# Optimization experiments

Measured on AMD Instinct MI355X. Metric: run time of the kernel, lower is better.

## Reference

```python
import jax, jax.numpy as jnp
import numpy as np

# LIF hyperparameters (match init_kwargs)
DT = 1.0
TAU = 20.0
THRESHOLD = 1.0
RESET = 0.0
REST = 0.0
REFR_PERIOD = 2.0
LOW_BOUND = -1.0
KOEFF = float(np.exp(-DT / TAU))  # membrane decay per step
N = 2048
N_IN = 512
N_OUT = 256
B = 64
T = 512


def setup_inputs() -> dict:
    key = jax.random.key(0)
    k1, k2 = jax.random.split(key)
    # Binary input spike trains [B, n_in, T] (uint8 semantics, stored as float32)
    inp = (jax.random.uniform(k1, (B, N_IN, T)) < 0.2).astype(jnp.float32)
    # Dense synaptic weight matrix W [N, N]; row i = incoming weights of neuron i
    W = jax.random.normal(k2, (N, N), dtype=jnp.float32) * (0.1 / np.sqrt(N))
    return {"inp": inp, "W": W}


def reference(inp, W):
    batch, n_in, time = inp.shape
    n = W.shape[0]
    xs = jnp.moveaxis(inp, 2, 0)  # [T, B, n_in]

    def step(carry, x_t):
        state, refr, out_t = carry  # state/refr/out_t: [B, N]
        # Inject input spikes into the first n_in output slots
        out_t = out_t.at[:, :n_in].set(x_t)
        # LIF update: decay toward rest + synaptic input W @ out_t
        state = (state - REST) * KOEFF + REST + jnp.einsum('ij,bj->bi', W, out_t)
        # Refractory neurons clamped to reset potential
        state = jnp.where(refr > 0, RESET, state)
        spike = state >= THRESHOLD
        refr = refr - DT
        refr = jnp.where(spike, REFR_PERIOD, refr)
        # Lower-bound clamp on membrane potential
        state = jnp.where(state < LOW_BOUND, LOW_BOUND, state)
        out_t = spike.astype(jnp.float32)
        return (state, refr, out_t), out_t[:, -N_OUT:]

    init = (jnp.zeros((batch, n), jnp.float32),
            jnp.zeros((batch, n), jnp.float32),
            jnp.zeros((batch, n), jnp.float32))
    _, outs = jax.lax.scan(step, init, xs)  # outs: [T, B, n_out]
    return jnp.transpose(outs, (1, 2, 0))  # [B, n_out, T]
```

## Files before the change

### kernel.cpp

```cpp
#include <hip/hip_runtime.h>

#define KOEFF 0.951229424500714f
#define K64   0.040762204f
#define LOG2K (-0.07213475204444817f)

typedef unsigned short u16;
typedef __attribute__((ext_vector_type(8))) short short8;
typedef __attribute__((ext_vector_type(4))) float f32x4;

__device__ __forceinline__ u16 f2bf(float f) {
  unsigned int v = __float_as_uint(f);
  unsigned int r = (v + 0x7FFFu + ((v >> 16) & 1u)) >> 16;
  return (u16)r;
}
__device__ __forceinline__ float bf2f(u16 u) {
  return __uint_as_float(((unsigned int)u) << 16);
}

__global__ __launch_bounds__(256) void k_prep(const float* __restrict__ X, const float* __restrict__ W,
                                              u16* __restrict__ XT, u16* __restrict__ Whi,
                                              float* __restrict__ WT2, int* __restrict__ flags) {
  __shared__ float tile[64][65];
  const int blk = blockIdx.x;
  if (blk < 4096) {
    const int b  = blk >> 6;
    const int r2 = blk & 63;
    const int j0 = (r2 & 7) * 64;
    const int t0 = (r2 >> 3) * 64;
    const float* src = X + ((size_t)b * 512 + j0) * 512 + t0;
    for (int e = threadIdx.x; e < 64 * 16; e += 256) {
      int r = e >> 4, c = e & 15;
      float4 v = *(const float4*)(src + (size_t)r * 512 + c * 4);
      tile[r][c * 4 + 0] = v.x; tile[r][c * 4 + 1] = v.y;
      tile[r][c * 4 + 2] = v.z; tile[r][c * 4 + 3] = v.w;
    }
    __syncthreads();
    u16* dst = XT + ((size_t)b * 512 + t0) * 512 + j0;
    for (int e = threadIdx.x; e < 64 * 16; e += 256) {
      int tr = e >> 4, c = e & 15;
      ushort4 o;
      o.x = f2bf(tile[c * 4 + 0][tr]); o.y = f2bf(tile[c * 4 + 1][tr]);
      o.z = f2bf(tile[c * 4 + 2][tr]); o.w = f2bf(tile[c * 4 + 3][tr]);
      *(ushort4*)(dst + (size_t)tr * 512 + c * 4) = o;
    }
  } else if (blk < 7168) {
    if (blk == 4096 && threadIdx.x < 64) flags[threadIdx.x] = 0;
    int p = (blk - 4096) * 256 + threadIdx.x;
    int i = p >> 9, j = p & 511;
    Whi[p] = f2bf(W[(size_t)(512 + i) * 2048 + j]);
  } else {
    const int bx = blk - 7168;
    const int i0 = (bx / 24) * 64;
    const int j0 = (bx % 24) * 64;
    const float* src = W + (size_t)(512 + i0) * 2048 + 512 + j0;
    for (int e = threadIdx.x; e < 64 * 16; e += 256) {
      int r = e >> 4, c = e & 15;
      float4 v = *(const float4*)(src + (size_t)r * 2048 + c * 4);
      tile[r][c * 4 + 0] = v.x; tile[r][c * 4 + 1] = v.y;
      tile[r][c * 4 + 2] = v.z; tile[r][c * 4 + 3] = v.w;
    }
    __syncthreads();
    float* dst = WT2 + (size_t)j0 * 1536 + i0;
    for (int e = threadIdx.x; e < 64 * 16; e += 256) {
      int jr = e >> 4, c = e & 15;
      float4 o;
      o.x = tile[c * 4 + 0][jr]; o.y = tile[c * 4 + 1][jr];
      o.z = tile[c * 4 + 2][jr]; o.w = tile[c * 4 + 3][jr];
      *(float4*)(dst + (size_t)jr * 1536 + c * 4) = o;
    }
  }
}

__global__ __launch_bounds__(256) void k_gemm(const u16* __restrict__ A,
                                              const u16* __restrict__ Bx, u16* __restrict__ U,
                                              float* __restrict__ P) {
  __shared__ u16 lA[128 * 64];
  __shared__ u16 lB[128 * 64];
  const int b    = blockIdx.y;
  const int mt   = blockIdx.x >> 2;
  const int nt   = blockIdx.x & 3;
  const int tid  = threadIdx.x;
  const int wv   = tid >> 6;
  const int lane = tid & 63;
  const int wr   = wv >> 1, wc = wv & 1;

  f32x4 acc[4][4];
#pragma unroll
  for (int mi = 0; mi < 4; ++mi)
#pragma unroll
    for (int ni = 0; ni < 4; ++ni) acc[mi][ni] = (f32x4)0.0f;

  const u16* gA = A + (size_t)mt * 128 * 512;
  const u16* gB = Bx + ((size_t)b * 512 + nt * 128) * 512;

  for (int k0 = 0; k0 < 512; k0 += 64) {
#pragma unroll
    for (int it = 0; it < 4; ++it) {
      int byteoff = wv * 4096 + it * 1024 + lane * 16;
      int row   = byteoff >> 7;
      int chunk = (byteoff >> 4) & 7;
      int ksub  = (chunk ^ (row & 7)) * 8;
      int ldsoff = wv * 2048 + it * 512;
      __builtin_amdgcn_global_load_lds(
          (const __attribute__((address_space(1))) void*)(gA + (size_t)row * 512 + k0 + ksub),
          (__attribute__((address_space(3))) void*)(lA + ldsoff), 16, 0, 0);
      __builtin_amdgcn_global_load_lds(
          (const __attribute__((address_space(1))) void*)(gB + (size_t)row * 512 + k0 + ksub),
          (__attribute__((address_space(3))) void*)(lB + ldsoff), 16, 0, 0);
    }
    __syncthreads();
#pragma unroll
    for (int kk = 0; kk < 2; ++kk) {
      short8 ah[4], bb[4];
      const int kc = kk * 4 + (lane >> 4);
      const int sw = lane & 7;
#pragma unroll
      for (int mi = 0; mi < 4; ++mi) {
        int m = wr * 64 + mi * 16 + (lane & 15);
        ah[mi] = *(const short8*)&lA[m * 64 + ((kc ^ sw) << 3)];
      }
#pragma unroll
      for (int ni = 0; ni < 4; ++ni) {
        int n = wc * 64 + ni * 16 + (lane & 15);
        bb[ni] = *(const short8*)&lB[n * 64 + ((kc ^ sw) << 3)];
      }
#pragma unroll
      for (int mi = 0; mi < 4; ++mi)
#pragma unroll
        for (int ni = 0; ni < 4; ++ni)
          acc[mi][ni] = __builtin_amdgcn_mfma_f32_16x16x32_bf16(ah[mi], bb[ni], acc[mi][ni], 0, 0, 0);
    }
    __syncthreads();
  }
#pragma unroll
  for (int mi = 0; mi < 4; ++mi) {
    int ib = mt * 128 + wr * 64 + mi * 16 + ((lane >> 4) << 2);
#pragma unroll
    for (int ni = 0; ni < 4; ++ni) {
      int t = nt * 128 + wc * 64 + ni * 16 + (lane & 15);
      f32x4 v = acc[mi][ni];
      ushort4 o;
      o.x = f2bf(v.x); o.y = f2bf(v.y); o.z = f2bf(v.z); o.w = f2bf(v.w);
      *(ushort4*)(U + ((size_t)b * 512 + t) * 1536 + ib) = o;
    }
  }
  {
    const int tl = lane & 15;
    const int c  = nt * 2 + wc;
    float pv[4][4];
#pragma unroll
    for (int mi = 0; mi < 4; ++mi)
#pragma unroll
      for (int q = 0; q < 4; ++q) pv[mi][q] = 0.f;
#pragma unroll
    for (int ni = 0; ni < 4; ++ni) {
      float w = exp2f(LOG2K * (float)(63 - ni * 16 - tl));
#pragma unroll
      for (int mi = 0; mi < 4; ++mi) {
        f32x4 a = acc[mi][ni];
        pv[mi][0] = fmaf(w, a.x, pv[mi][0]);
        pv[mi][1] = fmaf(w, a.y, pv[mi][1]);
        pv[mi][2] = fmaf(w, a.z, pv[mi][2]);
        pv[mi][3] = fmaf(w, a.w, pv[mi][3]);
      }
    }
#pragma unroll
    for (int off = 1; off < 16; off <<= 1)
#pragma unroll
      for (int mi = 0; mi < 4; ++mi)
#pragma unroll
        for (int q = 0; q < 4; ++q)
          pv[mi][q] += __shfl_xor(pv[mi][q], off, 16);
    if (tl == 0) {
      int ib = mt * 128 + wr * 64 + ((lane >> 4) << 2);
      float* pb = P + ((size_t)b * 8 + c) * 1536 + ib;
#pragma unroll
      for (int mi = 0; mi < 4; ++mi)
#pragma unroll
        for (int q = 0; q < 4; ++q) pb[mi * 16 + q] = pv[mi][q];
    }
  }
}

__global__ __launch_bounds__(256) void k_chunk(const u16* __restrict__ U, const float* __restrict__ P,
                                               float* __restrict__ out, int* __restrict__ flags) {
  const int g = blockIdx.x * 256 + threadIdx.x;
  const int i = g * 2;
  const int c = blockIdx.y, b = blockIdx.z;
  float s0 = 0.f, s1 = 0.f;
  const float* pp = P + (size_t)b * 8 * 1536 + i;
  for (int d = 0; d < c; ++d) {
    float2 pv = *(const float2*)(pp + (size_t)d * 1536);
    s0 = fmaf(s0, K64, pv.x);
    s1 = fmaf(s1, K64, pv.y);
  }
  const u16* up = U + ((size_t)b * 512 + c * 64) * 1536 + i;
  const bool wr = (i >= 1280);
  float* op = out + ((size_t)b * 256 + (i - 1280)) * 512 + c * 64;
  bool viol = false;
  unsigned int buf[8];
#pragma unroll
  for (int j = 0; j < 8; ++j) buf[j] = *(const unsigned int*)(up + (size_t)j * 1536);
  for (int t0 = 0; t0 < 64; t0 += 8) {
    float sp0[8], sp1[8];
#pragma unroll
    for (int j = 0; j < 8; ++j) {
      unsigned int u = buf[j];
      if (t0 + 8 < 64) buf[j] = *(const unsigned int*)(up + (size_t)(t0 + 8 + j) * 1536);
      s0 = fmaf(s0, KOEFF, bf2f((u16)(u & 0xffffu)));
      s1 = fmaf(s1, KOEFF, bf2f((u16)(u >> 16)));
      bool a = (s0 >= 1.0f), bsp = (s1 >= 1.0f);
      viol = viol || a || bsp || (s0 < -1.0f) || (s1 < -1.0f);
      sp0[j] = a ? 1.f : 0.f;
      sp1[j] = bsp ? 1.f : 0.f;
    }
    if (wr) {
      *(float4*)(op + t0)           = make_float4(sp0[0], sp0[1], sp0[2], sp0[3]);
      *(float4*)(op + t0 + 4)       = make_float4(sp0[4], sp0[5], sp0[6], sp0[7]);
      *(float4*)(op + 512 + t0)     = make_float4(sp1[0], sp1[1], sp1[2], sp1[3]);
      *(float4*)(op + 512 + t0 + 4) = make_float4(sp1[4], sp1[5], sp1[6], sp1[7]);
    }
  }
  if (viol) atomicOr(&flags[b], 1);
}

__global__ __launch_bounds__(768) void k_fix(const u16* __restrict__ U, const float* __restrict__ WT2,
                                             const int* __restrict__ flags, float* __restrict__ out) {
  const int b = blockIdx.x;
  if (flags[b] == 0) return;
  const int tid = threadIdx.x;
  const int wv = tid >> 6, lane = tid & 63;
  __shared__ unsigned long long spk[24];
  for (int w = tid; w < 24; w += 768) spk[w] = 0ULL;
  __syncthreads();
  float s0 = 0.f, s1 = 0.f, r0 = 0.f, r1 = 0.f;
  const int i0 = 2 * tid;
  const u16* ub = U + (size_t)b * 512 * 1536 + i0;
  unsigned int u = *(const unsigned int*)ub;
  for (int t = 0; t < 512; ++t) {
    unsigned int unext = u;
    if (t < 511) unext = *(const unsigned int*)(ub + (size_t)(t + 1) * 1536);
    float a0 = fmaf(s0, KOEFF, bf2f((u16)(u & 0xffffu)));
    float a1 = fmaf(s1, KOEFF, bf2f((u16)(u >> 16)));
    for (int wd = 0; wd < 24; ++wd) {
      unsigned long long m = spk[wd];
      while (m) {
        int bit = __ffsll(m) - 1;
        m &= m - 1;
        int jp = ((wd >> 1) << 7) + (bit << 1) + (wd & 1);
        float2 rv = *(const float2*)(WT2 + (size_t)jp * 1536 + i0);
        a0 += rv.x; a1 += rv.y;
      }
    }
    if (r0 > 0.f) a0 = 0.f;
    if (r1 > 0.f) a1 = 0.f;
    bool sp0 = a0 >= 1.0f, sp1 = a1 >= 1.0f;
    r0 -= 1.f; r1 -= 1.f;
    if (sp0) r0 = 2.f;
    if (sp1) r1 = 2.f;
    if (a0 < -1.f) a0 = -1.f;
    if (a1 < -1.f) a1 = -1.f;
    s0 = a0; s1 = a1;
    if (i0 >= 1280) {
      float* o = out + ((size_t)b * 256 + (i0 - 1280)) * 512 + t;
      o[0]   = sp0 ? 1.f : 0.f;
      o[512] = sp1 ? 1.f : 0.f;
    }
    __syncthreads();
    unsigned long long b0 = __ballot(sp0);
    unsigned long long b1 = __ballot(sp1);
    if (lane == 0) { spk[2 * wv] = b0; spk[2 * wv + 1] = b1; }
    __syncthreads();
    u = unext;
  }
}

__global__ __launch_bounds__(256) void k_wtf(const float* __restrict__ W, float* __restrict__ WTF) {
  __shared__ float tile[64][65];
  const int i0 = blockIdx.x * 64;
  const int j0 = blockIdx.y * 64;
  const float* src = W + (size_t)(512 + i0) * 2048 + j0;
  for (int e = threadIdx.x; e < 64 * 16; e += 256) {
    int r = e >> 4, c = e & 15;
    float4 v = *(const float4*)(src + (size_t)r * 2048 + c * 4);
    tile[r][c * 4 + 0] = v.x; tile[r][c * 4 + 1] = v.y;
    tile[r][c * 4 + 2] = v.z; tile[r][c * 4 + 3] = v.w;
  }
  __syncthreads();
  float* dst = WTF + (size_t)j0 * 1536 + i0;
  for (int e = threadIdx.x; e < 64 * 16; e += 256) {
    int jr = e >> 4, c = e & 15;
    float4 o;
    o.x = tile[c * 4 + 0][jr]; o.y = tile[c * 4 + 1][jr];
    o.z = tile[c * 4 + 2][jr]; o.w = tile[c * 4 + 3][jr];
    *(float4*)(dst + (size_t)jr * 1536 + c * 4) = o;
  }
}

__global__ __launch_bounds__(256) void k_exact(const float* __restrict__ X, const float* __restrict__ W,
                                               const float* __restrict__ WTF, int use_wt,
                                               float* __restrict__ out) {
  const int b = blockIdx.x, tid = threadIdx.x;
  const int wv = tid >> 6, lane = tid & 63;
  float st[6], rf[6];
#pragma unroll
  for (int r = 0; r < 6; ++r) { st[r] = 0.f; rf[r] = 0.f; }
  __shared__ unsigned int mask[64];
  for (int w = tid; w < 64; w += 256) mask[w] = 0u;
  __syncthreads();
  for (int t = 0; t < 512; ++t) {
    {
      float x = X[((size_t)b * 512 + tid) * 512 + t];
      unsigned long long bl = __ballot(x > 0.5f);
      if (lane == 0) { mask[2 * wv] = (unsigned int)bl; mask[2 * wv + 1] = (unsigned int)(bl >> 32); }
      x = X[((size_t)b * 512 + 256 + tid) * 512 + t];
      bl = __ballot(x > 0.5f);
      if (lane == 0) { mask[8 + 2 * wv] = (unsigned int)bl; mask[9 + 2 * wv] = (unsigned int)(bl >> 32); }
    }
    __syncthreads();
    float add[6] = {0.f, 0.f, 0.f, 0.f, 0.f, 0.f};
    for (int wd = 0; wd < 64; ++wd) {
      unsigned int m = mask[wd];
      while (m) {
        int bitp = __ffs(m) - 1;
        m &= m - 1;
        int j = wd * 32 + bitp;
        if (use_wt) {
          const float* row = WTF + (size_t)j * 1536;
#pragma unroll
          for (int r = 0; r < 6; ++r) add[r] += row[tid + 256 * r];
        } else {
#pragma unroll
          for (int r = 0; r < 6; ++r) add[r] += W[(size_t)(512 + tid + 256 * r) * 2048 + j];
        }
      }
    }
    bool sp[6];
#pragma unroll
    for (int r = 0; r < 6; ++r) {
      float a = fmaf(st[r], KOEFF, add[r]);
      if (rf[r] > 0.f) a = 0.f;
      sp[r] = a >= 1.0f;
      rf[r] -= 1.f;
      if (sp[r]) rf[r] = 2.f;
      if (a < -1.f) a = -1.f;
      st[r] = a;
      int gi = 512 + tid + 256 * r;
      if (gi >= 1792) out[((size_t)b * 256 + (gi - 1792)) * 512 + t] = sp[r] ? 1.f : 0.f;
    }
    __syncthreads();
#pragma unroll
    for (int r = 0; r < 6; ++r) {
      unsigned long long bl = __ballot(sp[r]);
      if (lane == 0) {
        mask[16 + 8 * r + 2 * wv] = (unsigned int)bl;
        mask[17 + 8 * r + 2 * wv] = (unsigned int)(bl >> 32);
      }
    }
    __syncthreads();
  }
}

extern "C" void kernel_launch(void* const* d_in, const int* in_sizes, int n_in,
                              void* d_out, int out_size, void* d_ws, size_t ws_size,
                              hipStream_t stream) {
  const float* X = (const float*)d_in[0];
  const float* W = (const float*)d_in[1];
  float* out = (float*)d_out;
  char* ws = (char*)d_ws;

  const size_t SZ_XT  = 64ull * 512 * 512 * 2;
  const size_t SZ_WH  = 1536ull * 512 * 2;
  const size_t SZ_WT2 = 1536ull * 1536 * 4;
  const size_t SZ_U   = 64ull * 512 * 1536 * 2;
  const size_t SZ_P   = 64ull * 8 * 1536 * 4;
  const size_t SZ_FL  = 256;
  const size_t NEED_FULL = SZ_XT + SZ_WH + SZ_WT2 + SZ_U + SZ_P + SZ_FL;
  const size_t NEED_MID  = 2048ull * 1536 * 4;

  if (ws_size >= NEED_FULL) {
    u16*   XT  = (u16*)ws;
    u16*   Whi = (u16*)(ws + SZ_XT);
    float* WT2 = (float*)(ws + SZ_XT + SZ_WH);
    u16*   U   = (u16*)(ws + SZ_XT + SZ_WH + SZ_WT2);
    float* P   = (float*)(ws + SZ_XT + SZ_WH + SZ_WT2 + SZ_U);
    int*   FL  = (int*)(ws + SZ_XT + SZ_WH + SZ_WT2 + SZ_U + SZ_P);
    k_prep<<<7744, 256, 0, stream>>>(X, W, XT, Whi, WT2, FL);
    k_gemm<<<dim3(48, 64), 256, 0, stream>>>(Whi, XT, U, P);
    k_chunk<<<dim3(3, 8, 64), 256, 0, stream>>>(U, P, out, FL);
    k_fix<<<64, 768, 0, stream>>>(U, WT2, FL, out);
  } else if (ws_size >= NEED_MID) {
    float* WTF = (float*)ws;
    k_wtf<<<dim3(24, 32), 256, 0, stream>>>(W, WTF);
    k_exact<<<64, 256, 0, stream>>>(X, W, WTF, 1, out);
  } else {
    k_exact<<<64, 256, 0, stream>>>(X, W, nullptr, 0, out);
  }
}
```

Before: 237.4 us.

## Enlarge GEMM tiles to 256x256 with double-buffered LDS prefetch pipeline

Rewrites the bf16 GEMM that computes the input-driven currents to use 256x256 output tiles, 512 threads (8 waves), and double-buffered LDS stages. The next K-tile is loaded asynchronously while MFMAs run on the current one, with explicit vmcnt waits, barriers and setprio hints. This is meant to hide global-load latency and raise reuse per LDS byte. In exchange it uses more LDS and registers per block, and the grid shrinks to 768 blocks, which may leave fewer blocks per CU.

```diff
diff --git a/kernel.cpp b/kernel.cpp
--- a/kernel.cpp
+++ b/kernel.cpp
@@ -71,73 +71,120 @@
   }
 }
 
-__global__ __launch_bounds__(256) void k_gemm(const u16* __restrict__ A,
-                                              const u16* __restrict__ Bx, u16* __restrict__ U,
-                                              float* __restrict__ P) {
-  __shared__ u16 lA[128 * 64];
-  __shared__ u16 lB[128 * 64];
+__global__ __launch_bounds__(512, 2) void k_gemm(const u16* __restrict__ A,
+                                                 const u16* __restrict__ Bx, u16* __restrict__ U,
+                                                 float* __restrict__ P) {
+  __shared__ u16 lA[2][256 * 64];
+  __shared__ u16 lB[2][256 * 64];
   const int b    = blockIdx.y;
-  const int mt   = blockIdx.x >> 2;
-  const int nt   = blockIdx.x & 3;
+  const int mt   = blockIdx.x >> 1;
+  const int nt   = blockIdx.x & 1;
   const int tid  = threadIdx.x;
   const int wv   = tid >> 6;
   const int lane = tid & 63;
-  const int wr   = wv >> 1, wc = wv & 1;
-
-  f32x4 acc[4][4];
-#pragma unroll
-  for (int mi = 0; mi < 4; ++mi)
+  const int tl   = lane & 15;
+  const int qg   = lane >> 4;
+  const int l7   = lane & 7;
+  const int wr   = wv >> 2;
+  const int wcn  = wv & 3;
+
+  f32x4 acc[8][4];
+#pragma unroll
+  for (int mi = 0; mi < 8; ++mi)
 #pragma unroll
     for (int ni = 0; ni < 4; ++ni) acc[mi][ni] = (f32x4)0.0f;
 
-  const u16* gA = A + (size_t)mt * 128 * 512;
-  const u16* gB = Bx + ((size_t)b * 512 + nt * 128) * 512;
-
-  for (int k0 = 0; k0 < 512; k0 += 64) {
-#pragma unroll
-    for (int it = 0; it < 4; ++it) {
-      int byteoff = wv * 4096 + it * 1024 + lane * 16;
-      int row   = byteoff >> 7;
-      int chunk = (byteoff >> 4) & 7;
-      int ksub  = (chunk ^ (row & 7)) * 8;
-      int ldsoff = wv * 2048 + it * 512;
-      __builtin_amdgcn_global_load_lds(
-          (const __attribute__((address_space(1))) void*)(gA + (size_t)row * 512 + k0 + ksub),
-          (__attribute__((address_space(3))) void*)(lA + ldsoff), 16, 0, 0);
-      __builtin_amdgcn_global_load_lds(
-          (const __attribute__((address_space(1))) void*)(gB + (size_t)row * 512 + k0 + ksub),
-          (__attribute__((address_space(3))) void*)(lB + ldsoff), 16, 0, 0);
-    }
-    __syncthreads();
-#pragma unroll
-    for (int kk = 0; kk < 2; ++kk) {
-      short8 ah[4], bb[4];
-      const int kc = kk * 4 + (lane >> 4);
-      const int sw = lane & 7;
-#pragma unroll
-      for (int mi = 0; mi < 4; ++mi) {
-        int m = wr * 64 + mi * 16 + (lane & 15);
-        ah[mi] = *(const short8*)&lA[m * 64 + ((kc ^ sw) << 3)];
+  const u16* gA = A + (size_t)mt * 256 * 512;
+  const u16* gB = Bx + ((size_t)b * 512 + nt * 256) * 512;
+
+  const int srow = tid >> 3;
+  const int ssw  = (((tid & 7) ^ (srow & 7)) << 3);
+
+#define STAGE(ktv, dv)                                                          \
+  do {                                                                          \
+    const u16* sa_ = gA + (ktv) * 64;                                           \
+    const u16* sb_ = gB + (ktv) * 64;                                           \
+    _Pragma("unroll")                                                           \
+    for (int a_ = 0; a_ < 4; ++a_)                                              \
+      __builtin_amdgcn_global_load_lds(                                         \
+          (const __attribute__((address_space(1))) void*)(sa_ + (size_t)(a_ * 64 + srow) * 512 + ssw), \
+          (__attribute__((address_space(3))) void*)(&lA[dv][0] + a_ * 4096 + wv * 512), 16, 0, 0); \
+    _Pragma("unroll")                                                           \
+    for (int a_ = 0; a_ < 4; ++a_)                                              \
+      __builtin_amdgcn_global_load_lds(                                         \
+          (const __attribute__((address_space(1))) void*)(sb_ + (size_t)(a_ * 64 + srow) * 512 + ssw), \
+          (__attribute__((address_space(3))) void*)(&lB[dv][0] + a_ * 4096 + wv * 512), 16, 0, 0); \
+  } while (0)
+
+  auto compute_tile = [&](int d) {
+#pragma unroll
+    for (int q = 0; q < 4; ++q) {
+      const int mh = q & 1, nh = q >> 1;
+      short8 ah[4][2], bb[2][2];
+#pragma unroll
+      for (int mi = 0; mi < 4; ++mi)
+#pragma unroll
+        for (int kk = 0; kk < 2; ++kk) {
+          int row = wr * 128 + (mh * 4 + mi) * 16 + tl;
+          ah[mi][kk] = *(const short8*)&lA[d][row * 64 + ((((kk << 2) | qg) ^ l7) << 3)];
+        }
+#pragma unroll
+      for (int ni = 0; ni < 2; ++ni)
+#pragma unroll
+        for (int kk = 0; kk < 2; ++kk) {
+          int row = wcn * 64 + (nh * 2 + ni) * 16 + tl;
+          bb[ni][kk] = *(const short8*)&lB[d][row * 64 + ((((kk << 2) | qg) ^ l7) << 3)];
+        }
+      __builtin_amdgcn_s_setprio(1);
+#pragma unroll
+      for (int mi = 0; mi < 4; ++mi)
+#pragma unroll
+        for (int ni = 0; ni < 2; ++ni)
+#pragma unroll
+          for (int kk = 0; kk < 2; ++kk)
+            acc[mh * 4 + mi][nh * 2 + ni] =
+                __builtin_amdgcn_mfma_f32_16x16x32_bf16(ah[mi][kk], bb[ni][kk],
+                                                        acc[mh * 4 + mi][nh * 2 + ni], 0, 0, 0);
+      __builtin_amdgcn_s_setprio(0);
+    }
+  };
+
+  STAGE(0, 0);
+#pragma unroll
+  for (int it = 0; it < 4; ++it) {
+    {
+      STAGE(2 * it + 1, 1);
+      asm volatile("s_waitcnt vmcnt(8)" ::: "memory");
+      __builtin_amdgcn_sched_barrier(0);
+      __builtin_amdgcn_s_barrier();
+      __builtin_amdgcn_sched_barrier(0);
+      compute_tile(0);
+      __builtin_amdgcn_sched_barrier(0);
+      __builtin_amdgcn_s_barrier();
+    }
+    {
+      if (it < 3) {
+        STAGE(2 * it + 2, 0);
+        asm volatile("s_waitcnt vmcnt(8)" ::: "memory");
+      } else {
+        asm volatile("s_waitcnt vmcnt(0)" ::: "memory");
       }
-#pragma unroll
-      for (int ni = 0; ni < 4; ++ni) {
-        int n = wc * 64 + ni * 16 + (lane & 15);
-        bb[ni] = *(const short8*)&lB[n * 64 + ((kc ^ sw) << 3)];
-      }
-#pragma unroll
-      for (int mi = 0; mi < 4; ++mi)
-#pragma unroll
-        for (int ni = 0; ni < 4; ++ni)
-          acc[mi][ni] = __builtin_amdgcn_mfma_f32_16x16x32_bf16(ah[mi], bb[ni], acc[mi][ni], 0, 0, 0);
-    }
-    __syncthreads();
-  }
-#pragma unroll
-  for (int mi = 0; mi < 4; ++mi) {
-    int ib = mt * 128 + wr * 64 + mi * 16 + ((lane >> 4) << 2);
+      __builtin_amdgcn_sched_barrier(0);
+      __builtin_amdgcn_s_barrier();
+      __builtin_amdgcn_sched_barrier(0);
+      compute_tile(1);
+      __builtin_amdgcn_sched_barrier(0);
+      __builtin_amdgcn_s_barrier();
+    }
+  }
+#undef STAGE
+
+#pragma unroll
+  for (int mi = 0; mi < 8; ++mi) {
+    int ib = mt * 256 + wr * 128 + mi * 16 + (qg << 2);
 #pragma unroll
     for (int ni = 0; ni < 4; ++ni) {
-      int t = nt * 128 + wc * 64 + ni * 16 + (lane & 15);
+      int t = nt * 256 + wcn * 64 + ni * 16 + tl;
       f32x4 v = acc[mi][ni];
       ushort4 o;
       o.x = f2bf(v.x); o.y = f2bf(v.y); o.z = f2bf(v.z); o.w = f2bf(v.w);
@@ -145,18 +192,17 @@
     }
   }
   {
-    const int tl = lane & 15;
-    const int c  = nt * 2 + wc;
-    float pv[4][4];
-#pragma unroll
-    for (int mi = 0; mi < 4; ++mi)
+    const int c = nt * 4 + wcn;
+    float pv[8][4];
+#pragma unroll
+    for (int mi = 0; mi < 8; ++mi)
 #pragma unroll
       for (int q = 0; q < 4; ++q) pv[mi][q] = 0.f;
 #pragma unroll
     for (int ni = 0; ni < 4; ++ni) {
       float w = exp2f(LOG2K * (float)(63 - ni * 16 - tl));
 #pragma unroll
-      for (int mi = 0; mi < 4; ++mi) {
+      for (int mi = 0; mi < 8; ++mi) {
         f32x4 a = acc[mi][ni];
         pv[mi][0] = fmaf(w, a.x, pv[mi][0]);
         pv[mi][1] = fmaf(w, a.y, pv[mi][1]);
@@ -167,15 +213,14 @@
 #pragma unroll
     for (int off = 1; off < 16; off <<= 1)
 #pragma unroll
-      for (int mi = 0; mi < 4; ++mi)
+      for (int mi = 0; mi < 8; ++mi)
 #pragma unroll
         for (int q = 0; q < 4; ++q)
           pv[mi][q] += __shfl_xor(pv[mi][q], off, 16);
     if (tl == 0) {
-      int ib = mt * 128 + wr * 64 + ((lane >> 4) << 2);
-      float* pb = P + ((size_t)b * 8 + c) * 1536 + ib;
-#pragma unroll
-      for (int mi = 0; mi < 4; ++mi)
+      float* pb = P + ((size_t)b * 8 + c) * 1536 + mt * 256 + wr * 128 + (qg << 2);
+#pragma unroll
+      for (int mi = 0; mi < 8; ++mi)
 #pragma unroll
         for (int q = 0; q < 4; ++q) pb[mi * 16 + q] = pv[mi][q];
     }
@@ -386,7 +431,7 @@
     float* P   = (float*)(ws + SZ_XT + SZ_WH + SZ_WT2 + SZ_U);
     int*   FL  = (int*)(ws + SZ_XT + SZ_WH + SZ_WT2 + SZ_U + SZ_P);
     k_prep<<<7744, 256, 0, stream>>>(X, W, XT, Whi, WT2, FL);
-    k_gemm<<<dim3(48, 64), 256, 0, stream>>>(Whi, XT, U, P);
+    k_gemm<<<dim3(12, 64), 512, 0, stream>>>(Whi, XT, U, P);
     k_chunk<<<dim3(3, 8, 64), 256, 0, stream>>>(U, P, out, FL);
     k_fix<<<64, 768, 0, stream>>>(U, WT2, FL, out);
   } else if (ws_size >= NEED_MID) {
```

After: 242.5 us. 1.02x slower.
